# Performance work log

Measured on AMD Instinct MI355X. Metric: run time of the kernel, lower is better.

Reference implementation:

```python
import jax, jax.numpy as jnp
import numpy as np

jax.config.update("jax_enable_x64", True)

B, H, W = 16384, 19, 19
MAX_FLOOD = min(H * W // 4, 100)  # = 90, as in the torch module


def _count_neighbors(m):
    # m: [B,H,W] float. Sum of 4 orthogonal neighbors (zero-padded edges).
    up = jnp.pad(m[:, :-1, :], ((0, 0), (1, 0), (0, 0)))
    down = jnp.pad(m[:, 1:, :], ((0, 0), (0, 1), (0, 0)))
    left = jnp.pad(m[:, :, :-1], ((0, 0), (0, 0), (1, 0)))
    right = jnp.pad(m[:, :, 1:], ((0, 0), (0, 0), (0, 1)))
    return up + down + left + right


def _dilate(m):
    # m: [B,H,W] bool. OR of 4 orthogonal neighbors (False-padded edges).
    up = jnp.pad(m[:, :-1, :], ((0, 0), (1, 0), (0, 0)))
    down = jnp.pad(m[:, 1:, :], ((0, 0), (0, 1), (0, 0)))
    left = jnp.pad(m[:, :, :-1], ((0, 0), (0, 0), (1, 0)))
    right = jnp.pad(m[:, :, 1:], ((0, 0), (0, 0), (0, 1)))
    return up | down | left | right


def _flood_fill(seeds, mask):
    # Iterative neighbor expansion within mask, bounded iters + early exit.
    def cond(st):
        _, changed, i = st
        return changed & (i < MAX_FLOOD)

    def body(st):
        g, _, i = st
        exp = _dilate(g) & mask & ~g
        return (g | exp, exp.any(), i + 1)

    g, _, _ = jax.lax.while_loop(cond, body, (seeds, seeds.any(), jnp.int32(0)))
    return g


def setup_inputs() -> dict:
    key = jax.random.key(0)
    k1, k2, k3, k4, k5, k6 = jax.random.split(key, 6)
    # 0 = empty, 1 = black, 2 = white (planes never overlap)
    board = jax.random.randint(k1, (B, H, W), 0, 3)
    stones = jnp.stack([board == 1, board == 2], axis=1).astype(jnp.float32)
    current_player = jax.random.randint(k2, (B,), 0, 2).astype(jnp.int32)
    ko_rc = jax.random.randint(k3, (B, 2), 0, H).astype(jnp.int32)
    has_ko = jax.random.uniform(k4, (B,)) < 0.25
    ko_points = jnp.where(has_ko[:, None], ko_rc, jnp.int32(-1))
    hmax = np.iinfo(np.int64).max
    zobrist_stones = jax.random.randint(k5, (2, H, W), 0, hmax, dtype=jnp.int64)
    zobrist_turn = jax.random.randint(k6, (2,), 0, hmax, dtype=jnp.int64)
    position_hash = jnp.zeros((B,), jnp.int64)
    return {
        "stones": stones,
        "current_player": current_player,
        "ko_points": ko_points,
        "zobrist_stones": zobrist_stones,
        "zobrist_turn": zobrist_turn,
        "position_hash": position_hash,
    }


def reference(stones, current_player, ko_points, zobrist_stones, zobrist_turn, position_hash):
    stones_b = stones > 0.5                       # [B,2,H,W] bool
    empty_f = 1.0 - stones.sum(axis=1)            # [B,H,W] float (0/1)
    empty = ~stones_b.any(axis=1)                 # empty_mask
    liberties = _count_neighbors(empty_f)         # float liberty count per point

    # legal = empty points with at least one empty neighbor
    legal = empty & (liberties > 0.0)

    # capture moves: opponent stones with exactly one liberty
    cp = current_player.astype(jnp.int32)
    opp = jnp.take_along_axis(stones_b, (1 - cp)[:, None, None, None], axis=1)[:, 0]
    vulnerable = opp & (jnp.round(liberties).astype(jnp.int32) == 1)
    cap = empty & (_count_neighbors(vulnerable.astype(jnp.float32)) > 0.0)
    legal = legal | cap

    # ko restriction: mask the single ko point per game (if set)
    valid_ko = ko_points[:, 0] >= 0
    r_eq = jnp.arange(H)[None, :, None] == ko_points[:, 0][:, None, None]
    c_eq = jnp.arange(W)[None, None, :] == ko_points[:, 1][:, None, None]
    legal = legal & ~(valid_ko[:, None, None] & r_eq & c_eq)

    # flood fill the full groups-in-atari within opponent stones
    groups = _flood_fill(vulnerable, opp)

    # zobrist hash: XOR of stone hashes over the board + turn toggle
    contrib = jnp.where(stones_b, zobrist_stones[None], jnp.int64(0))  # [B,2,H,W]
    board_hash = jax.lax.reduce(contrib, np.int64(0), jax.lax.bitwise_xor, (1, 2, 3))
    new_hash = position_hash ^ board_hash ^ zobrist_turn[cp] ^ zobrist_turn[1 - cp]

    return (liberties, legal, groups, new_hash)
```

## Files before the change

kernel.cpp:

```cpp
#include <hip/hip_runtime.h>
#include <stdint.h>

#define WW 19
#define NP 361
#define M19 0x7FFFFu
#define BPW 3
#define NWAVES 4
#define BPB 12
#define TPB 256
#define CHF (BPB * 722)
#define CH4 (CHF / 4)
#define BMW 272
#define PLSTR 97

typedef float f32x4 __attribute__((ext_vector_type(4)));

__device__ __forceinline__ uint32_t rev19(uint32_t x) { return __brev(x) >> 13; }

__device__ __forceinline__ uint32_t runfill(uint32_t g, uint32_t m) {
  const uint32_t up = g | (m & ((m + g) ^ m ^ g));
  const uint32_t rm = rev19(m);
  const uint32_t rg = rev19(g);
  const uint32_t dn = rg | (rm & ((rm + rg) ^ rm ^ rg));
  return up | rev19(dn);
}

__global__ __launch_bounds__(TPB, 4) void go_fused(
    const float* __restrict__ stones, const int* __restrict__ cur,
    const int* __restrict__ ko, const int* __restrict__ zob,
    const int* __restrict__ zturn, const int* __restrict__ phash,
    float* __restrict__ out, int B) {
  __shared__ uint32_t bmp[BMW];
  __shared__ uint32_t pl[BPB * PLSTR];

  const int wid = threadIdx.x >> 6;
  const int lane = threadIdx.x & 63;
  const int b0 = blockIdx.x * BPB;
  const int nb = min(BPB, B - b0);
  const size_t NB = (size_t)B * NP;

  int zb[6], zw[6];
#pragma unroll
  for (int i = 0; i < 6; ++i) {
    const int p = i * 64 + lane;
    zb[i] = (p < NP) ? zob[p] : 0;
    zw[i] = (p < NP) ? zob[NP + p] : 0;
  }
  const int zt = zturn[0] ^ zturn[1];

  {
    const f32x4* src = (const f32x4*)(stones + (size_t)b0 * 722);
    const int nf4 = nb * 722 / 4;
    for (int j = 0; j < (CH4 + TPB - 1) / TPB; ++j) {
      const int q = threadIdx.x + TPB * j;
      uint32_t m = 0;
      if (q < nf4) {
        const f32x4 v = src[q];
        m = (uint32_t)(v.x > 0.5f) | ((uint32_t)(v.y > 0.5f) << 1) |
            ((uint32_t)(v.z > 0.5f) << 2) | ((uint32_t)(v.w > 0.5f) << 3);
      }
      uint32_t x = m | ((uint32_t)__shfl_xor((int)m, 1, 64) << 4);
      x = x | ((uint32_t)__shfl_xor((int)x, 2, 64) << 8);
      x = x | ((uint32_t)__shfl_xor((int)x, 4, 64) << 16);
      if ((lane & 7) == 0 && q < CH4) bmp[q >> 3] = x;
    }
  }
  __syncthreads();

  {
    int hv[BPW];
#pragma unroll
    for (int k = 0; k < BPW; ++k) {
      const int lb = wid * BPW + k;
      const uint32_t base = lb * 722;
      int h = 0;
#pragma unroll
      for (int i = 0; i < 6; ++i) {
        const int cc = i * 64 + lane;
        if (cc < NP) {
          uint32_t pos = base + cc;
          uint32_t s = (bmp[pos >> 5] >> (pos & 31)) & 1u;
          h ^= zb[i] & -(int)s;
          pos = base + 361 + cc;
          s = (bmp[pos >> 5] >> (pos & 31)) & 1u;
          h ^= zw[i] & -(int)s;
        }
      }
      hv[k] = h;
    }
#pragma unroll
    for (int off = 32; off > 0; off >>= 1) {
#pragma unroll
      for (int k = 0; k < BPW; ++k) hv[k] ^= __shfl_xor(hv[k], off, 64);
    }
    if (lane == 0) {
#pragma unroll
      for (int k = 0; k < BPW; ++k) {
        const int b = b0 + wid * BPW + k;
        if (b < B) out[3 * NB + b] = (float)(phash[b] ^ hv[k] ^ zt);
      }
    }
  }

  {
    const int k = (lane * 27) >> 9;
    const int r = lane - k * WW;
    const int lb = wid * BPW + k;
    const int b = b0 + lb;
    const bool vl = (lane < 57) && (lb < nb);
    const int lbs = vl ? lb : 0;

    uint32_t brow, wrow;
    {
      const uint32_t base = (uint32_t)lbs * 722 + (uint32_t)r * WW;
      const uint32_t d = base >> 5, sh = base & 31;
      const uint64_t w = ((uint64_t)bmp[d + 1] << 32) | bmp[d];
      brow = (uint32_t)(w >> sh) & M19;
      const uint32_t base2 = base + 361;
      const uint32_t d2 = base2 >> 5, sh2 = base2 & 31;
      const uint64_t w2 = ((uint64_t)bmp[d2 + 1] << 32) | bmp[d2];
      wrow = (uint32_t)(w2 >> sh2) & M19;
    }
    const int cp = vl ? cur[b] : 0;
    int2 kk = {-1, -1};
    if (vl) kk = ((const int2*)ko)[b];
    uint32_t mrow = (cp == 0) ? wrow : brow;
    uint32_t erow = ~(brow | wrow) & M19;
    if (!vl) { mrow = 0; erow = 0; }

    uint32_t t;
    t = __shfl(erow, lane - 1, 64);
    const uint32_t eu = (r > 0) ? t : 0u;
    t = __shfl(erow, lane + 1, 64);
    const uint32_t ed = (r < 18) ? t : 0u;
    const uint32_t el = (erow << 1) & M19;
    const uint32_t er_ = erow >> 1;
    const uint32_t s1 = eu ^ ed, c1 = eu & ed;
    const uint32_t s2 = el ^ er_, c2 = el & er_;
    const uint32_t cc = s1 & s2;
    const uint32_t L0 = s1 ^ s2;
    const uint32_t L1 = c1 ^ c2 ^ cc;
    const uint32_t L2 = (c1 & c2) | (cc & (c1 | c2));
    uint32_t leg = erow & (eu | ed | el | er_);
    const uint32_t vul = mrow & L0 & ~L1;
    t = __shfl(vul, lane - 1, 64);
    const uint32_t vu = (r > 0) ? t : 0u;
    t = __shfl(vul, lane + 1, 64);
    const uint32_t vd = (r < 18) ? t : 0u;
    leg |= erow & (vu | vd | ((vul << 1) & M19) | (vul >> 1));
    if (kk.x == r) leg &= ~(1u << kk.y);

    uint32_t g = runfill(vul, mrow);
    for (int it = 0; it < 90; ++it) {
      t = __shfl(g, lane - 1, 64);
      const uint32_t gu = (r > 0) ? t : 0u;
      t = __shfl(g, lane + 1, 64);
      const uint32_t gd = (r < 18) ? t : 0u;
      const uint32_t gn = runfill(g | ((gu | gd) & mrow), mrow);
      if (!__any(gn != g)) break;
      g = gn;
    }

    if (vl) {
      uint32_t* pb = &pl[lb * PLSTR];
      pb[r] = L0;
      pb[19 + r] = L1;
      pb[38 + r] = L2;
      pb[57 + r] = leg;
      pb[76 + r] = g;
    }
  }
  __syncthreads();

  {
    const int nq = nb * NP / 4;
    f32x4* s0 = (f32x4*)(out + (size_t)b0 * NP);
    f32x4* s1 = (f32x4*)(out + NB + (size_t)b0 * NP);
    f32x4* s2 = (f32x4*)(out + 2 * NB + (size_t)b0 * NP);
    for (int q = threadIdx.x; q < nq; q += TPB) {
      f32x4 t0, t1, t2;
#pragma unroll
      for (int j = 0; j < 4; ++j) {
        const int id = q * 4 + j;
        const int lb = (int)(((uint64_t)id * 5948986ull) >> 31);
        const int p = id - lb * NP;
        const int r = (p * 27) >> 9;
        const int c = p - r * WW;
        const uint32_t* pb = &pl[lb * PLSTR];
        const uint32_t l0 = (pb[r] >> c) & 1u;
        const uint32_t l1 = (pb[19 + r] >> c) & 1u;
        const uint32_t l2 = (pb[38 + r] >> c) & 1u;
        t0[j] = (float)(l0 + 2u * l1 + 4u * l2);
        t1[j] = (float)((pb[57 + r] >> c) & 1u);
        t2[j] = (float)((pb[76 + r] >> c) & 1u);
      }
      __builtin_nontemporal_store(t0, &s0[q]);
      __builtin_nontemporal_store(t1, &s1[q]);
      __builtin_nontemporal_store(t2, &s2[q]);
    }
    const int rem0 = nq * 4;
    for (int id = rem0 + threadIdx.x; id < nb * NP; id += TPB) {
      const int lb = (int)(((uint64_t)id * 5948986ull) >> 31);
      const int p = id - lb * NP;
      const int r = (p * 27) >> 9;
      const int c = p - r * WW;
      const uint32_t* pb = &pl[lb * PLSTR];
      const uint32_t l0 = (pb[r] >> c) & 1u;
      const uint32_t l1 = (pb[19 + r] >> c) & 1u;
      const uint32_t l2 = (pb[38 + r] >> c) & 1u;
      out[(size_t)b0 * NP + id] = (float)(l0 + 2u * l1 + 4u * l2);
      out[NB + (size_t)b0 * NP + id] = (float)((pb[57 + r] >> c) & 1u);
      out[2 * NB + (size_t)b0 * NP + id] = (float)((pb[76 + r] >> c) & 1u);
    }
  }
}

extern "C" void kernel_launch(void* const* d_in, const int* in_sizes, int n_in,
                              void* d_out, int out_size, void* d_ws,
                              size_t ws_size, hipStream_t stream) {
  const float* stones = (const float*)d_in[0];
  const int* cur = (const int*)d_in[1];
  const int* ko = (const int*)d_in[2];
  const int* zob = (const int*)d_in[3];
  const int* zturn = (const int*)d_in[4];
  const int* phash = (const int*)d_in[5];
  float* out = (float*)d_out;

  const int B = in_sizes[0] / (2 * NP);
  const int blocks = (B + BPB - 1) / BPB;
  go_fused<<<blocks, TPB, 0, stream>>>(stones, cur, ko, zob, zturn, phash, out,
                                       B);
}
```

Before: 30.35 us.

## Shrink blocks to one wave of three boards and drop block barriers

Each workgroup is now a single 64-lane wave handling three boards. Both __syncthreads barriers are removed and shared memory shrinks, with the bitmap packed via float2 loads and wave shuffles. The output phase switches from float4 nontemporal stores to scalar per-element stores, looping over positions and boards. The aim is to avoid barrier stalls and uneven flood-fill wait across four waves, at the cost of many more small blocks and narrower store instructions. Correctness relies on the hardware's wave-level lockstep in place of explicit barriers when writing and reading shared memory.

```diff
diff --git a/kernel.cpp b/kernel.cpp
--- a/kernel.cpp
+++ b/kernel.cpp
@@ -4,16 +4,10 @@
 #define WW 19
 #define NP 361
 #define M19 0x7FFFFu
-#define BPW 3
-#define NWAVES 4
-#define BPB 12
-#define TPB 256
-#define CHF (BPB * 722)
-#define CH4 (CHF / 4)
-#define BMW 272
+#define BPB 3
+#define TPB 64
 #define PLSTR 97
-
-typedef float f32x4 __attribute__((ext_vector_type(4)));
+#define BMW 69
 
 __device__ __forceinline__ uint32_t rev19(uint32_t x) { return __brev(x) >> 13; }
 
@@ -25,7 +19,7 @@
   return up | rev19(dn);
 }
 
-__global__ __launch_bounds__(TPB, 4) void go_fused(
+__global__ __launch_bounds__(TPB, 4) void go_wave(
     const float* __restrict__ stones, const int* __restrict__ cur,
     const int* __restrict__ ko, const int* __restrict__ zob,
     const int* __restrict__ zturn, const int* __restrict__ phash,
@@ -33,8 +27,7 @@
   __shared__ uint32_t bmp[BMW];
   __shared__ uint32_t pl[BPB * PLSTR];
 
-  const int wid = threadIdx.x >> 6;
-  const int lane = threadIdx.x & 63;
+  const int lane = threadIdx.x;
   const int b0 = blockIdx.x * BPB;
   const int nb = min(BPB, B - b0);
   const size_t NB = (size_t)B * NP;
@@ -49,70 +42,61 @@
   const int zt = zturn[0] ^ zturn[1];
 
   {
-    const f32x4* src = (const f32x4*)(stones + (size_t)b0 * 722);
-    const int nf4 = nb * 722 / 4;
-    for (int j = 0; j < (CH4 + TPB - 1) / TPB; ++j) {
-      const int q = threadIdx.x + TPB * j;
+    const float2* src = (const float2*)(stones + (size_t)b0 * 722);
+    const int nf2 = nb * 361;
+#pragma unroll
+    for (int j = 0; j < 17; ++j) {
+      const int q = j * 64 + lane;
       uint32_t m = 0;
-      if (q < nf4) {
-        const f32x4 v = src[q];
-        m = (uint32_t)(v.x > 0.5f) | ((uint32_t)(v.y > 0.5f) << 1) |
-            ((uint32_t)(v.z > 0.5f) << 2) | ((uint32_t)(v.w > 0.5f) << 3);
+      if (q < nf2) {
+        const float2 v = src[q];
+        m = (uint32_t)(v.x > 0.5f) | ((uint32_t)(v.y > 0.5f) << 1);
       }
-      uint32_t x = m | ((uint32_t)__shfl_xor((int)m, 1, 64) << 4);
-      x = x | ((uint32_t)__shfl_xor((int)x, 2, 64) << 8);
-      x = x | ((uint32_t)__shfl_xor((int)x, 4, 64) << 16);
-      if ((lane & 7) == 0 && q < CH4) bmp[q >> 3] = x;
+      uint32_t x = m | ((uint32_t)__shfl_xor((int)m, 1, 64) << 2);
+      x |= (uint32_t)__shfl_xor((int)x, 2, 64) << 4;
+      x |= (uint32_t)__shfl_xor((int)x, 4, 64) << 8;
+      x |= (uint32_t)__shfl_xor((int)x, 8, 64) << 16;
+      if ((lane & 15) == 0) bmp[j * 4 + (lane >> 4)] = x;
     }
   }
-  __syncthreads();
 
   {
-    int hv[BPW];
+    int hv0 = 0, hv1 = 0, hv2 = 0;
 #pragma unroll
-    for (int k = 0; k < BPW; ++k) {
-      const int lb = wid * BPW + k;
-      const uint32_t base = lb * 722;
-      int h = 0;
-#pragma unroll
-      for (int i = 0; i < 6; ++i) {
-        const int cc = i * 64 + lane;
-        if (cc < NP) {
-          uint32_t pos = base + cc;
-          uint32_t s = (bmp[pos >> 5] >> (pos & 31)) & 1u;
-          h ^= zb[i] & -(int)s;
-          pos = base + 361 + cc;
-          s = (bmp[pos >> 5] >> (pos & 31)) & 1u;
-          h ^= zw[i] & -(int)s;
-        }
+    for (int i = 0; i < 6; ++i) {
+      const int cc = i * 64 + lane;
+      if (cc < NP) {
+        uint32_t pos, s;
+        pos = cc;        s = (bmp[pos >> 5] >> (pos & 31)) & 1u; hv0 ^= zb[i] & -(int)s;
+        pos = cc + 361;  s = (bmp[pos >> 5] >> (pos & 31)) & 1u; hv0 ^= zw[i] & -(int)s;
+        pos = cc + 722;  s = (bmp[pos >> 5] >> (pos & 31)) & 1u; hv1 ^= zb[i] & -(int)s;
+        pos = cc + 1083; s = (bmp[pos >> 5] >> (pos & 31)) & 1u; hv1 ^= zw[i] & -(int)s;
+        pos = cc + 1444; s = (bmp[pos >> 5] >> (pos & 31)) & 1u; hv2 ^= zb[i] & -(int)s;
+        pos = cc + 1805; s = (bmp[pos >> 5] >> (pos & 31)) & 1u; hv2 ^= zw[i] & -(int)s;
       }
-      hv[k] = h;
     }
 #pragma unroll
     for (int off = 32; off > 0; off >>= 1) {
-#pragma unroll
-      for (int k = 0; k < BPW; ++k) hv[k] ^= __shfl_xor(hv[k], off, 64);
+      hv0 ^= __shfl_xor(hv0, off, 64);
+      hv1 ^= __shfl_xor(hv1, off, 64);
+      hv2 ^= __shfl_xor(hv2, off, 64);
     }
-    if (lane == 0) {
-#pragma unroll
-      for (int k = 0; k < BPW; ++k) {
-        const int b = b0 + wid * BPW + k;
-        if (b < B) out[3 * NB + b] = (float)(phash[b] ^ hv[k] ^ zt);
-      }
+    if (lane < nb) {
+      const int h = (lane == 0) ? hv0 : (lane == 1) ? hv1 : hv2;
+      out[3 * NB + b0 + lane] = (float)(phash[b0 + lane] ^ h ^ zt);
     }
   }
 
   {
     const int k = (lane * 27) >> 9;
     const int r = lane - k * WW;
-    const int lb = wid * BPW + k;
-    const int b = b0 + lb;
-    const bool vl = (lane < 57) && (lb < nb);
-    const int lbs = vl ? lb : 0;
+    const int b = b0 + k;
+    const bool vl = (lane < 57) && (k < nb);
+    const int ks = vl ? k : 0;
 
     uint32_t brow, wrow;
     {
-      const uint32_t base = (uint32_t)lbs * 722 + (uint32_t)r * WW;
+      const uint32_t base = (uint32_t)ks * 722 + (uint32_t)r * WW;
       const uint32_t d = base >> 5, sh = base & 31;
       const uint64_t w = ((uint64_t)bmp[d + 1] << 32) | bmp[d];
       brow = (uint32_t)(w >> sh) & M19;
@@ -162,7 +146,7 @@
     }
 
     if (vl) {
-      uint32_t* pb = &pl[lb * PLSTR];
+      uint32_t* pb = &pl[k * PLSTR];
       pb[r] = L0;
       pb[19 + r] = L1;
       pb[38 + r] = L2;
@@ -170,47 +154,27 @@
       pb[76 + r] = g;
     }
   }
-  __syncthreads();
 
   {
-    const int nq = nb * NP / 4;
-    f32x4* s0 = (f32x4*)(out + (size_t)b0 * NP);
-    f32x4* s1 = (f32x4*)(out + NB + (size_t)b0 * NP);
-    f32x4* s2 = (f32x4*)(out + 2 * NB + (size_t)b0 * NP);
-    for (int q = threadIdx.x; q < nq; q += TPB) {
-      f32x4 t0, t1, t2;
 #pragma unroll
-      for (int j = 0; j < 4; ++j) {
-        const int id = q * 4 + j;
-        const int lb = (int)(((uint64_t)id * 5948986ull) >> 31);
-        const int p = id - lb * NP;
-        const int r = (p * 27) >> 9;
-        const int c = p - r * WW;
-        const uint32_t* pb = &pl[lb * PLSTR];
-        const uint32_t l0 = (pb[r] >> c) & 1u;
-        const uint32_t l1 = (pb[19 + r] >> c) & 1u;
-        const uint32_t l2 = (pb[38 + r] >> c) & 1u;
-        t0[j] = (float)(l0 + 2u * l1 + 4u * l2);
-        t1[j] = (float)((pb[57 + r] >> c) & 1u);
-        t2[j] = (float)((pb[76 + r] >> c) & 1u);
+    for (int j = 0; j < 6; ++j) {
+      const int p = j * 64 + lane;
+      const bool ok = p < NP;
+      const int r = ok ? ((p * 27) >> 9) : 0;
+      const int c = p - r * WW;
+#pragma unroll
+      for (int k = 0; k < BPB; ++k) {
+        if (ok && k < nb) {
+          const uint32_t* pb = &pl[k * PLSTR];
+          const uint32_t l0 = (pb[r] >> c) & 1u;
+          const uint32_t l1 = (pb[19 + r] >> c) & 1u;
+          const uint32_t l2 = (pb[38 + r] >> c) & 1u;
+          const size_t o = (size_t)(b0 + k) * NP + p;
+          out[o] = (float)(l0 + 2u * l1 + 4u * l2);
+          out[NB + o] = (float)((pb[57 + r] >> c) & 1u);
+          out[2 * NB + o] = (float)((pb[76 + r] >> c) & 1u);
+        }
       }
-      __builtin_nontemporal_store(t0, &s0[q]);
-      __builtin_nontemporal_store(t1, &s1[q]);
-      __builtin_nontemporal_store(t2, &s2[q]);
-    }
-    const int rem0 = nq * 4;
-    for (int id = rem0 + threadIdx.x; id < nb * NP; id += TPB) {
-      const int lb = (int)(((uint64_t)id * 5948986ull) >> 31);
-      const int p = id - lb * NP;
-      const int r = (p * 27) >> 9;
-      const int c = p - r * WW;
-      const uint32_t* pb = &pl[lb * PLSTR];
-      const uint32_t l0 = (pb[r] >> c) & 1u;
-      const uint32_t l1 = (pb[19 + r] >> c) & 1u;
-      const uint32_t l2 = (pb[38 + r] >> c) & 1u;
-      out[(size_t)b0 * NP + id] = (float)(l0 + 2u * l1 + 4u * l2);
-      out[NB + (size_t)b0 * NP + id] = (float)((pb[57 + r] >> c) & 1u);
-      out[2 * NB + (size_t)b0 * NP + id] = (float)((pb[76 + r] >> c) & 1u);
     }
   }
 }
@@ -228,6 +192,6 @@
 
   const int B = in_sizes[0] / (2 * NP);
   const int blocks = (B + BPB - 1) / BPB;
-  go_fused<<<blocks, TPB, 0, stream>>>(stones, cur, ko, zob, zturn, phash, out,
-                                       B);
+  go_wave<<<blocks, TPB, 0, stream>>>(stones, cur, ko, zob, zturn, phash, out,
+                                      B);
 }
```

Result: faster. 29.37 us (-3.2%).

## Stage raw stone floats into LDS via direct global-to-LDS loads

Applied to the files above, without the earlier changes.

Replaces the register load plus shuffle-based bit packing of the stone planes with direct global_load_lds transfers of the raw floats into a larger shared staging buffer. The hash and row extraction then read floats from LDS and threshold them per cell. This is meant to remove VGPR round-trips and shuffle packing from the load phase, at the cost of about 35KB of LDS per block, which may cut occupancy, and 19 LDS reads per row to build the bitmasks.

```diff
diff --git a/kernel.cpp b/kernel.cpp
--- a/kernel.cpp
+++ b/kernel.cpp
@@ -8,9 +8,7 @@
 #define NWAVES 4
 #define BPB 12
 #define TPB 256
-#define CHF (BPB * 722)
-#define CH4 (CHF / 4)
-#define BMW 272
+#define STGF (BPB * 722)
 #define PLSTR 97
 
 typedef float f32x4 __attribute__((ext_vector_type(4)));
@@ -30,7 +28,7 @@
     const int* __restrict__ ko, const int* __restrict__ zob,
     const int* __restrict__ zturn, const int* __restrict__ phash,
     float* __restrict__ out, int B) {
-  __shared__ uint32_t bmp[BMW];
+  __shared__ float stg[STGF];
   __shared__ uint32_t pl[BPB * PLSTR];
 
   const int wid = threadIdx.x >> 6;
@@ -49,20 +47,19 @@
   const int zt = zturn[0] ^ zturn[1];
 
   {
-    const f32x4* src = (const f32x4*)(stones + (size_t)b0 * 722);
-    const int nf4 = nb * 722 / 4;
-    for (int j = 0; j < (CH4 + TPB - 1) / TPB; ++j) {
-      const int q = threadIdx.x + TPB * j;
-      uint32_t m = 0;
-      if (q < nf4) {
-        const f32x4 v = src[q];
-        m = (uint32_t)(v.x > 0.5f) | ((uint32_t)(v.y > 0.5f) << 1) |
-            ((uint32_t)(v.z > 0.5f) << 2) | ((uint32_t)(v.w > 0.5f) << 3);
-      }
-      uint32_t x = m | ((uint32_t)__shfl_xor((int)m, 1, 64) << 4);
-      x = x | ((uint32_t)__shfl_xor((int)x, 2, 64) << 8);
-      x = x | ((uint32_t)__shfl_xor((int)x, 4, 64) << 16);
-      if ((lane & 7) == 0 && q < CH4) bmp[q >> 3] = x;
+    const uint32_t nfl = (uint32_t)nb * 722u;
+    const float* gsrc = stones + (size_t)b0 * 722;
+#pragma unroll
+    for (int rnd = 0; rnd < 9; ++rnd) {
+      const uint32_t fo = (uint32_t)rnd * 1024u + (uint32_t)wid * 256u +
+                          (uint32_t)lane * 4u;
+      if (fo < nfl) {
+        __builtin_amdgcn_global_load_lds(
+            (const __attribute__((address_space(1))) uint32_t*)(gsrc + fo),
+            (__attribute__((address_space(3))) uint32_t*)(stg + rnd * 1024 +
+                                                          wid * 256),
+            16, 0, 0);
+      }
     }
   }
   __syncthreads();
@@ -72,18 +69,16 @@
 #pragma unroll
     for (int k = 0; k < BPW; ++k) {
       const int lb = wid * BPW + k;
-      const uint32_t base = lb * 722;
+      const int base = lb * 722;
       int h = 0;
 #pragma unroll
       for (int i = 0; i < 6; ++i) {
         const int cc = i * 64 + lane;
         if (cc < NP) {
-          uint32_t pos = base + cc;
-          uint32_t s = (bmp[pos >> 5] >> (pos & 31)) & 1u;
-          h ^= zb[i] & -(int)s;
-          pos = base + 361 + cc;
-          s = (bmp[pos >> 5] >> (pos & 31)) & 1u;
-          h ^= zw[i] & -(int)s;
+          const uint32_t sb = stg[base + cc] > 0.5f;
+          const uint32_t sw = stg[base + 361 + cc] > 0.5f;
+          h ^= zb[i] & -(int)sb;
+          h ^= zw[i] & -(int)sw;
         }
       }
       hv[k] = h;
@@ -110,16 +105,14 @@
     const bool vl = (lane < 57) && (lb < nb);
     const int lbs = vl ? lb : 0;
 
-    uint32_t brow, wrow;
+    uint32_t brow = 0, wrow = 0;
     {
-      const uint32_t base = (uint32_t)lbs * 722 + (uint32_t)r * WW;
-      const uint32_t d = base >> 5, sh = base & 31;
-      const uint64_t w = ((uint64_t)bmp[d + 1] << 32) | bmp[d];
-      brow = (uint32_t)(w >> sh) & M19;
-      const uint32_t base2 = base + 361;
-      const uint32_t d2 = base2 >> 5, sh2 = base2 & 31;
-      const uint64_t w2 = ((uint64_t)bmp[d2 + 1] << 32) | bmp[d2];
-      wrow = (uint32_t)(w2 >> sh2) & M19;
+      const float* rb = &stg[lbs * 722 + r * WW];
+#pragma unroll
+      for (int c = 0; c < WW; ++c) {
+        brow |= (uint32_t)(rb[c] > 0.5f) << c;
+        wrow |= (uint32_t)(rb[361 + c] > 0.5f) << c;
+      }
     }
     const int cp = vl ? cur[b] : 0;
     int2 kk = {-1, -1};
```

New measurement: 28.84 us. 1.05x faster.

## Split fused kernel into compute and expand kernels via workspace bitplanes

Applied to the files above, without the earlier changes.

When workspace is large enough, the fused kernel is split in two. The first kernel computes packed per-row bitplanes and the hash, and writes the bitplanes to global workspace. The second kernel reads those compact records into shared memory and expands them into float outputs using nontemporal stores. The aim is to decouple the flood-fill compute from the heavy output stores so each phase gets its own occupancy and schedule, at the cost of an extra launch and a workspace round trip. The fallback fused kernel is also rewritten to stage inputs into LDS with direct global-to-LDS loads instead of building a bitmap.

```diff
diff --git a/kernel.cpp b/kernel.cpp
--- a/kernel.cpp
+++ b/kernel.cpp
@@ -5,12 +5,12 @@
 #define NP 361
 #define M19 0x7FFFFu
 #define BPW 3
-#define NWAVES 4
 #define BPB 12
 #define TPB 256
-#define CHF (BPB * 722)
-#define CH4 (CHF / 4)
+#define CH4 (BPB * 722 / 4)
 #define BMW 272
+#define RSTR 96
+#define BPB2 16
 #define PLSTR 97
 
 typedef float f32x4 __attribute__((ext_vector_type(4)));
@@ -25,13 +25,12 @@
   return up | rev19(dn);
 }
 
-__global__ __launch_bounds__(TPB, 4) void go_fused(
+__global__ __launch_bounds__(TPB, 4) void k1_compute(
     const float* __restrict__ stones, const int* __restrict__ cur,
     const int* __restrict__ ko, const int* __restrict__ zob,
     const int* __restrict__ zturn, const int* __restrict__ phash,
-    float* __restrict__ out, int B) {
+    float* __restrict__ out, uint32_t* __restrict__ ws, int B) {
   __shared__ uint32_t bmp[BMW];
-  __shared__ uint32_t pl[BPB * PLSTR];
 
   const int wid = threadIdx.x >> 6;
   const int lane = threadIdx.x & 63;
@@ -162,6 +161,208 @@
     }
 
     if (vl) {
+      uint32_t* w = ws + (size_t)b * RSTR;
+      w[r] = L0;
+      w[19 + r] = L1;
+      w[38 + r] = L2;
+      w[57 + r] = leg;
+      w[76 + r] = g;
+    }
+  }
+}
+
+__global__ __launch_bounds__(TPB, 4) void k2_expand(
+    const uint32_t* __restrict__ ws, float* __restrict__ out, int B) {
+  __shared__ uint32_t rec[BPB2 * RSTR];
+
+  const int b0 = blockIdx.x * BPB2;
+  const int nb = min(BPB2, B - b0);
+  const size_t NB = (size_t)B * NP;
+
+  {
+    const uint4* src = (const uint4*)(ws + (size_t)b0 * RSTR);
+    uint4* dst = (uint4*)rec;
+#pragma unroll
+    for (int jj = 0; jj < 2; ++jj) {
+      const int q = threadIdx.x + TPB * jj;
+      if (q < BPB2 * RSTR / 4) dst[q] = src[q];
+    }
+  }
+  __syncthreads();
+
+  const int nq = nb * NP / 4;
+  f32x4* s0 = (f32x4*)(out + (size_t)b0 * NP);
+  f32x4* s1 = (f32x4*)(out + NB + (size_t)b0 * NP);
+  f32x4* s2 = (f32x4*)(out + 2 * NB + (size_t)b0 * NP);
+  for (int q = threadIdx.x; q < nq; q += TPB) {
+    f32x4 t0, t1, t2;
+#pragma unroll
+    for (int j = 0; j < 4; ++j) {
+      const int id = q * 4 + j;
+      const int lb = (int)(((uint64_t)id * 5948986ull) >> 31);
+      const int p = id - lb * NP;
+      const int r = (p * 27) >> 9;
+      const int c = p - r * WW;
+      const uint32_t* pb = &rec[lb * RSTR];
+      const uint32_t l0 = (pb[r] >> c) & 1u;
+      const uint32_t l1 = (pb[19 + r] >> c) & 1u;
+      const uint32_t l2 = (pb[38 + r] >> c) & 1u;
+      t0[j] = (float)(l0 + 2u * l1 + 4u * l2);
+      t1[j] = (float)((pb[57 + r] >> c) & 1u);
+      t2[j] = (float)((pb[76 + r] >> c) & 1u);
+    }
+    __builtin_nontemporal_store(t0, &s0[q]);
+    __builtin_nontemporal_store(t1, &s1[q]);
+    __builtin_nontemporal_store(t2, &s2[q]);
+  }
+  const int rem0 = nq * 4;
+  for (int id = rem0 + threadIdx.x; id < nb * NP; id += TPB) {
+    const int lb = (int)(((uint64_t)id * 5948986ull) >> 31);
+    const int p = id - lb * NP;
+    const int r = (p * 27) >> 9;
+    const int c = p - r * WW;
+    const uint32_t* pb = &rec[lb * RSTR];
+    const uint32_t l0 = (pb[r] >> c) & 1u;
+    const uint32_t l1 = (pb[19 + r] >> c) & 1u;
+    const uint32_t l2 = (pb[38 + r] >> c) & 1u;
+    out[(size_t)b0 * NP + id] = (float)(l0 + 2u * l1 + 4u * l2);
+    out[NB + (size_t)b0 * NP + id] = (float)((pb[57 + r] >> c) & 1u);
+    out[2 * NB + (size_t)b0 * NP + id] = (float)((pb[76 + r] >> c) & 1u);
+  }
+}
+
+__global__ __launch_bounds__(TPB, 4) void go_fused(
+    const float* __restrict__ stones, const int* __restrict__ cur,
+    const int* __restrict__ ko, const int* __restrict__ zob,
+    const int* __restrict__ zturn, const int* __restrict__ phash,
+    float* __restrict__ out, int B) {
+  __shared__ float stg[BPB * 722];
+  __shared__ uint32_t pl[BPB * PLSTR];
+
+  const int wid = threadIdx.x >> 6;
+  const int lane = threadIdx.x & 63;
+  const int b0 = blockIdx.x * BPB;
+  const int nb = min(BPB, B - b0);
+  const size_t NB = (size_t)B * NP;
+
+  int zb[6], zw[6];
+#pragma unroll
+  for (int i = 0; i < 6; ++i) {
+    const int p = i * 64 + lane;
+    zb[i] = (p < NP) ? zob[p] : 0;
+    zw[i] = (p < NP) ? zob[NP + p] : 0;
+  }
+  const int zt = zturn[0] ^ zturn[1];
+
+  {
+    const uint32_t nfl = (uint32_t)nb * 722u;
+    const float* gsrc = stones + (size_t)b0 * 722;
+#pragma unroll
+    for (int rnd = 0; rnd < 9; ++rnd) {
+      const uint32_t fo = (uint32_t)rnd * 1024u + (uint32_t)wid * 256u +
+                          (uint32_t)lane * 4u;
+      if (fo < nfl) {
+        __builtin_amdgcn_global_load_lds(
+            (const __attribute__((address_space(1))) uint32_t*)(gsrc + fo),
+            (__attribute__((address_space(3))) uint32_t*)(stg + rnd * 1024 +
+                                                          wid * 256),
+            16, 0, 0);
+      }
+    }
+  }
+  __syncthreads();
+
+  {
+    int hv[BPW];
+#pragma unroll
+    for (int k = 0; k < BPW; ++k) {
+      const int lb = wid * BPW + k;
+      const int base = lb * 722;
+      int h = 0;
+#pragma unroll
+      for (int i = 0; i < 6; ++i) {
+        const int cc = i * 64 + lane;
+        if (cc < NP) {
+          const uint32_t sb = stg[base + cc] > 0.5f;
+          const uint32_t sw = stg[base + 361 + cc] > 0.5f;
+          h ^= zb[i] & -(int)sb;
+          h ^= zw[i] & -(int)sw;
+        }
+      }
+      hv[k] = h;
+    }
+#pragma unroll
+    for (int off = 32; off > 0; off >>= 1) {
+#pragma unroll
+      for (int k = 0; k < BPW; ++k) hv[k] ^= __shfl_xor(hv[k], off, 64);
+    }
+    if (lane == 0) {
+#pragma unroll
+      for (int k = 0; k < BPW; ++k) {
+        const int b = b0 + wid * BPW + k;
+        if (b < B) out[3 * NB + b] = (float)(phash[b] ^ hv[k] ^ zt);
+      }
+    }
+  }
+
+  {
+    const int k = (lane * 27) >> 9;
+    const int r = lane - k * WW;
+    const int lb = wid * BPW + k;
+    const int b = b0 + lb;
+    const bool vl = (lane < 57) && (lb < nb);
+    const int lbs = vl ? lb : 0;
+
+    uint32_t brow = 0, wrow = 0;
+    {
+      const float* rb = &stg[lbs * 722 + r * WW];
+#pragma unroll
+      for (int c = 0; c < WW; ++c) {
+        brow |= (uint32_t)(rb[c] > 0.5f) << c;
+        wrow |= (uint32_t)(rb[361 + c] > 0.5f) << c;
+      }
+    }
+    const int cp = vl ? cur[b] : 0;
+    int2 kk = {-1, -1};
+    if (vl) kk = ((const int2*)ko)[b];
+    uint32_t mrow = (cp == 0) ? wrow : brow;
+    uint32_t erow = ~(brow | wrow) & M19;
+    if (!vl) { mrow = 0; erow = 0; }
+
+    uint32_t t;
+    t = __shfl(erow, lane - 1, 64);
+    const uint32_t eu = (r > 0) ? t : 0u;
+    t = __shfl(erow, lane + 1, 64);
+    const uint32_t ed = (r < 18) ? t : 0u;
+    const uint32_t el = (erow << 1) & M19;
+    const uint32_t er_ = erow >> 1;
+    const uint32_t s1 = eu ^ ed, c1 = eu & ed;
+    const uint32_t s2 = el ^ er_, c2 = el & er_;
+    const uint32_t cc = s1 & s2;
+    const uint32_t L0 = s1 ^ s2;
+    const uint32_t L1 = c1 ^ c2 ^ cc;
+    const uint32_t L2 = (c1 & c2) | (cc & (c1 | c2));
+    uint32_t leg = erow & (eu | ed | el | er_);
+    const uint32_t vul = mrow & L0 & ~L1;
+    t = __shfl(vul, lane - 1, 64);
+    const uint32_t vu = (r > 0) ? t : 0u;
+    t = __shfl(vul, lane + 1, 64);
+    const uint32_t vd = (r < 18) ? t : 0u;
+    leg |= erow & (vu | vd | ((vul << 1) & M19) | (vul >> 1));
+    if (kk.x == r) leg &= ~(1u << kk.y);
+
+    uint32_t g = runfill(vul, mrow);
+    for (int it = 0; it < 90; ++it) {
+      t = __shfl(g, lane - 1, 64);
+      const uint32_t gu = (r > 0) ? t : 0u;
+      t = __shfl(g, lane + 1, 64);
+      const uint32_t gd = (r < 18) ? t : 0u;
+      const uint32_t gn = runfill(g | ((gu | gd) & mrow), mrow);
+      if (!__any(gn != g)) break;
+      g = gn;
+    }
+
+    if (vl) {
       uint32_t* pb = &pl[lb * PLSTR];
       pb[r] = L0;
       pb[19 + r] = L1;
@@ -227,7 +428,16 @@
   float* out = (float*)d_out;
 
   const int B = in_sizes[0] / (2 * NP);
-  const int blocks = (B + BPB - 1) / BPB;
-  go_fused<<<blocks, TPB, 0, stream>>>(stones, cur, ko, zob, zturn, phash, out,
-                                       B);
+  const size_t need = (size_t)B * (RSTR * 4);
+
+  if (ws_size >= need) {
+    uint32_t* ws = (uint32_t*)d_ws;
+    k1_compute<<<(B + BPB - 1) / BPB, TPB, 0, stream>>>(stones, cur, ko, zob,
+                                                        zturn, phash, out, ws,
+                                                        B);
+    k2_expand<<<(B + BPB2 - 1) / BPB2, TPB, 0, stream>>>(ws, out, B);
+  } else {
+    go_fused<<<(B + BPB - 1) / BPB, TPB, 0, stream>>>(stones, cur, ko, zob,
+                                                      zturn, phash, out, B);
+  }
 }
```

After: 34.04 us. 12.2% more time.
